# Optimization experiments

Hardware: AMD Instinct MI355X
Metric: run time of the kernel (lower is better)

Reference implementation:

```python
import jax, jax.numpy as jnp
import numpy as np
import math

B, T, C = 2, 2048, 1024
N_HEADS = 16  # config.head_size in the original (actually number of heads)
HEAD_DIM = C // N_HEADS


def setup_inputs() -> dict:
    key = jax.random.key(0)
    k1, k2, k3 = jax.random.split(key, 3)
    s = 1.0 / math.sqrt(C)
    return {
        "x": jax.random.normal(k1, (B, T, C), dtype=jnp.float32),
        "W_attn": jax.random.normal(k2, (C, 3 * C), dtype=jnp.float32) * s,
        "b_attn": jnp.zeros((3 * C,), dtype=jnp.float32),
        "W_proj": jax.random.normal(k3, (C, C), dtype=jnp.float32) * s,
        "b_proj": jnp.zeros((C,), dtype=jnp.float32),
    }


def reference(x, W_attn, b_attn, W_proj, b_proj):
    Bsz, Tlen, Cdim = x.shape
    qkv = x @ W_attn + b_attn                      # [B,T,3C]
    q, k, v = jnp.split(qkv, 3, axis=-1)
    # [B,T,C] -> [B,H,T,D]
    def to_heads(t):
        return t.reshape(Bsz, Tlen, N_HEADS, HEAD_DIM).transpose(0, 2, 1, 3)
    q, k, v = to_heads(q), to_heads(k), to_heads(v)
    # NOTE: original multiplies by sqrt(head_dim) (faithful to source, not 1/sqrt)
    scale = jnp.asarray(math.sqrt(HEAD_DIM), dtype=x.dtype)
    att = jnp.einsum("bhqd,bhkd->bhqk", q, k) * scale
    causal = jnp.tril(jnp.ones((Tlen, Tlen), dtype=bool))
    att = jnp.where(causal[None, None, :, :], att, jnp.asarray(-jnp.inf, x.dtype))
    att = jax.nn.softmax(att, axis=-1)
    # dropout layers are identity in eval mode
    y = jnp.einsum("bhqk,bhkd->bhqd", att, v)
    y = y.transpose(0, 2, 1, 3).reshape(Bsz, Tlen, Cdim)
    return y @ W_proj + b_proj
```

## Files before the change

### kernel.cpp

```cpp
#include <hip/hip_runtime.h>
#include <hip/hip_bf16.h>


#define B_  2
#define T_  2048
#define C_  1024
#define H_  16
#define D_  64
#define M_  (B_ * T_)
#define N3_ (3 * C_)

typedef __attribute__((ext_vector_type(8))) short s16x8;
typedef __attribute__((ext_vector_type(4))) short s16x4;
typedef __attribute__((ext_vector_type(4))) float f32x4;

typedef const __attribute__((address_space(1))) unsigned int gu32_t;
typedef __attribute__((address_space(3))) unsigned int lu32_t;

__device__ __forceinline__ void gload_lds16(const short* g, short* l) {
    __builtin_amdgcn_global_load_lds((gu32_t*)g, (lu32_t*)l, 16, 0, 0);
}

__device__ __forceinline__ float b2f(unsigned short u) {
    return __uint_as_float(((unsigned)u) << 16);
}
__device__ __forceinline__ unsigned short f2b(float f) {
    unsigned u = __float_as_uint(f);
    return (unsigned short)((u + 0x7FFFu + ((u >> 16) & 1u)) >> 16);
}
__device__ __forceinline__ float fexp2(float x) {
#if __has_builtin(__builtin_amdgcn_exp2f)
    return __builtin_amdgcn_exp2f(x);
#else
    return exp2f(x);
#endif
}

__global__ __launch_bounds__(256) void cvt_split(
    const float* __restrict__ in, short* __restrict__ oh, short* __restrict__ ol, int n)
{
    int i = (blockIdx.x * 256 + threadIdx.x) * 8;
    if (i >= n) return;
    float4 a = *(const float4*)&in[i];
    float4 b = *(const float4*)&in[i + 4];
    float v[8] = {a.x, a.y, a.z, a.w, b.x, b.y, b.z, b.w};
    s16x8 h, l;
    #pragma unroll
    for (int j = 0; j < 8; j++) {
        unsigned short hb = f2b(v[j]);
        h[j] = (short)hb;
        l[j] = (short)f2b(v[j] - b2f(hb));
    }
    *(s16x8*)&oh[i] = h;
    *(s16x8*)&ol[i] = l;
}

__global__ __launch_bounds__(256) void cvtT_split(
    const float* __restrict__ in, short* __restrict__ oh, short* __restrict__ ol,
    int R, int Cn)
{
    __shared__ short th[64][80];
    __shared__ short tl[64][80];
    const int tid = threadIdx.x;
    const int k0 = blockIdx.y * 64;
    const int n0 = blockIdx.x * 64;
    {
        int rl = tid >> 4, cl = (tid & 15) * 4;
        #pragma unroll
        for (int i = 0; i < 4; i++) {
            int kr = rl + i * 16;
            float4 v4 = *(const float4*)&in[(size_t)(k0 + kr) * Cn + n0 + cl];
            float v[4] = {v4.x, v4.y, v4.z, v4.w};
            #pragma unroll
            for (int j = 0; j < 4; j++) {
                unsigned short hb = f2b(v[j]);
                th[cl + j][kr] = (short)hb;
                tl[cl + j][kr] = (short)f2b(v[j] - b2f(hb));
            }
        }
    }
    __syncthreads();
    {
        int ro = tid >> 2, co = (tid & 3) * 16;
        *(s16x8*)&oh[(size_t)(n0 + ro) * R + k0 + co]     = *(s16x8*)&th[ro][co];
        *(s16x8*)&oh[(size_t)(n0 + ro) * R + k0 + co + 8] = *(s16x8*)&th[ro][co + 8];
        *(s16x8*)&ol[(size_t)(n0 + ro) * R + k0 + co]     = *(s16x8*)&tl[ro][co];
        *(s16x8*)&ol[(size_t)(n0 + ro) * R + k0 + co + 8] = *(s16x8*)&tl[ro][co + 8];
    }
}

__global__ __launch_bounds__(256) void cvtT_bf16(
    const float* __restrict__ in, short* __restrict__ out, int R, int Cn)
{
    __shared__ short t[64][80];
    const int tid = threadIdx.x;
    const int k0 = blockIdx.y * 64;
    const int n0 = blockIdx.x * 64;
    {
        int rl = tid >> 4, cl = (tid & 15) * 4;
        #pragma unroll
        for (int i = 0; i < 4; i++) {
            int kr = rl + i * 16;
            float4 v = *(const float4*)&in[(size_t)(k0 + kr) * Cn + n0 + cl];
            t[cl + 0][kr] = (short)f2b(v.x);
            t[cl + 1][kr] = (short)f2b(v.y);
            t[cl + 2][kr] = (short)f2b(v.z);
            t[cl + 3][kr] = (short)f2b(v.w);
        }
    }
    __syncthreads();
    {
        int ro = tid >> 2, co = (tid & 3) * 16;
        *(s16x8*)&out[(size_t)(n0 + ro) * R + k0 + co]     = *(s16x8*)&t[ro][co];
        *(s16x8*)&out[(size_t)(n0 + ro) * R + k0 + co + 8] = *(s16x8*)&t[ro][co + 8];
    }
}

__global__ __launch_bounds__(256) void qkv_qk(
    const short* __restrict__ Ah, const short* __restrict__ Al,
    const short* __restrict__ BTh, const short* __restrict__ BTl,
    const float* __restrict__ bias,
    short* __restrict__ Qh, short* __restrict__ Ql,
    short* __restrict__ Kh, short* __restrict__ Kl)
{
    __shared__ short Ash[128 * 32], Asl[128 * 32];
    __shared__ short Bsh[128 * 32], Bsl[128 * 32];

    const int tid  = threadIdx.x;
    const int wave = tid >> 6, lane = tid & 63;
    const int wm = wave >> 1, wn = wave & 1;
    const int lm = lane & 15, lq = lane >> 4;
    const int m0 = blockIdx.y * 128, n0 = blockIdx.x * 128;
    const int gr = (lane >> 2);
    const int gc = (lane & 3) * 8;

    f32x4 acc[4][4] = {};

    for (int k0 = 0; k0 < C_; k0 += 32) {
        __syncthreads();
        #pragma unroll
        for (int j = 0; j < 2; j++) {
            int s = wave * 2 + j;
            int row = s * 16 + gr;
            size_t ga = (size_t)(m0 + row) * C_ + k0 + gc;
            size_t gb = (size_t)(n0 + row) * C_ + k0 + gc;
            gload_lds16(&Ah[ga],  &Ash[s * 512]);
            gload_lds16(&Al[ga],  &Asl[s * 512]);
            gload_lds16(&BTh[gb], &Bsh[s * 512]);
            gload_lds16(&BTl[gb], &Bsl[s * 512]);
        }
        __syncthreads();

        s16x8 ah[4], al[4], bh[4], bl[4];
        #pragma unroll
        for (int mi = 0; mi < 4; mi++) {
            int r = wm * 64 + mi * 16 + lm;
            ah[mi] = *(const s16x8*)&Ash[r * 32 + lq * 8];
            al[mi] = *(const s16x8*)&Asl[r * 32 + lq * 8];
        }
        #pragma unroll
        for (int nj = 0; nj < 4; nj++) {
            int r = wn * 64 + nj * 16 + lm;
            bh[nj] = *(const s16x8*)&Bsh[r * 32 + lq * 8];
            bl[nj] = *(const s16x8*)&Bsl[r * 32 + lq * 8];
        }
        #pragma unroll
        for (int mi = 0; mi < 4; mi++)
            #pragma unroll
            for (int nj = 0; nj < 4; nj++) {
                acc[mi][nj] = __builtin_amdgcn_mfma_f32_16x16x32_bf16(
                    ah[mi], bh[nj], acc[mi][nj], 0, 0, 0);
                acc[mi][nj] = __builtin_amdgcn_mfma_f32_16x16x32_bf16(
                    ah[mi], bl[nj], acc[mi][nj], 0, 0, 0);
                acc[mi][nj] = __builtin_amdgcn_mfma_f32_16x16x32_bf16(
                    al[mi], bh[nj], acc[mi][nj], 0, 0, 0);
            }
    }

    #pragma unroll
    for (int nj = 0; nj < 4; nj++) {
        int n = n0 + wn * 64 + nj * 16 + lm;
        float bv = bias[n];
        int isK = n >> 10;
        int c = n & (C_ - 1);
        int h = c >> 6, d = c & (D_ - 1);
        short* dh = isK ? Kh : Qh;
        short* dl = isK ? Kl : Ql;
        float scale = isK ? 1.0f : 11.541560327111708f;
        #pragma unroll
        for (int mi = 0; mi < 4; mi++) {
            #pragma unroll
            for (int r = 0; r < 4; r++) {
                int m  = m0 + wm * 64 + mi * 16 + lq * 4 + r;
                int bb = m >> 11, t = m & (T_ - 1);
                float v = (acc[mi][nj][r] + bv) * scale;
                size_t idx = (((size_t)bb * H_ + h) * T_ + t) * D_ + d;
                unsigned short hb = f2b(v);
                dh[idx] = (short)hb;
                dl[idx] = (short)f2b(v - b2f(hb));
            }
        }
    }
}

__global__ __launch_bounds__(256) void qkv_v(
    const short* __restrict__ Ah, const short* __restrict__ BTh,
    const float* __restrict__ bias, short* __restrict__ VT)
{
    __shared__ short Ash[128 * 32];
    __shared__ short Bsh[128 * 32];

    const int tid  = threadIdx.x;
    const int wave = tid >> 6, lane = tid & 63;
    const int wm = wave >> 1, wn = wave & 1;
    const int lm = lane & 15, lq = lane >> 4;
    const int m0 = blockIdx.y * 128, n0 = blockIdx.x * 128;
    const int gr = (lane >> 2);
    const int gc = (lane & 3) * 8;

    f32x4 acc[4][4] = {};

    for (int k0 = 0; k0 < C_; k0 += 32) {
        __syncthreads();
        #pragma unroll
        for (int j = 0; j < 2; j++) {
            int s = wave * 2 + j;
            int row = s * 16 + gr;
            gload_lds16(&Ah[(size_t)(m0 + row) * C_ + k0 + gc],  &Ash[s * 512]);
            gload_lds16(&BTh[(size_t)(n0 + row) * C_ + k0 + gc], &Bsh[s * 512]);
        }
        __syncthreads();

        s16x8 af[4], bfr[4];
        #pragma unroll
        for (int mi = 0; mi < 4; mi++)
            af[mi] = *(const s16x8*)&Ash[(wm * 64 + mi * 16 + lm) * 32 + lq * 8];
        #pragma unroll
        for (int nj = 0; nj < 4; nj++)
            bfr[nj] = *(const s16x8*)&Bsh[(wn * 64 + nj * 16 + lm) * 32 + lq * 8];
        #pragma unroll
        for (int mi = 0; mi < 4; mi++)
            #pragma unroll
            for (int nj = 0; nj < 4; nj++)
                acc[mi][nj] = __builtin_amdgcn_mfma_f32_16x16x32_bf16(
                    af[mi], bfr[nj], acc[mi][nj], 0, 0, 0);
    }

    #pragma unroll
    for (int nj = 0; nj < 4; nj++) {
        int n = n0 + wn * 64 + nj * 16 + lm;
        float bv = bias[n];
        int h = n >> 6, d = n & (D_ - 1);
        #pragma unroll
        for (int mi = 0; mi < 4; mi++) {
            #pragma unroll
            for (int r = 0; r < 4; r++) {
                int m  = m0 + wm * 64 + mi * 16 + lq * 4 + r;
                int bb = m >> 11, t = m & (T_ - 1);
                VT[(((size_t)bb * H_ + h) * D_ + d) * T_ + t] =
                    (short)f2b(acc[mi][nj][r] + bv);
            }
        }
    }
}

__global__ __launch_bounds__(256) void proj_mfma(
    const short* __restrict__ A, const short* __restrict__ BT,
    const float* __restrict__ bias, float* __restrict__ out)
{
    __shared__ short Ash[128 * 32];
    __shared__ short Bsh[128 * 32];

    const int tid  = threadIdx.x;
    const int wave = tid >> 6, lane = tid & 63;
    const int wm = wave >> 1, wn = wave & 1;
    const int lm = lane & 15, lq = lane >> 4;
    const int m0 = blockIdx.y * 128, n0 = blockIdx.x * 128;
    const int gr = (lane >> 2);
    const int gc = (lane & 3) * 8;

    f32x4 acc[4][4] = {};

    for (int k0 = 0; k0 < C_; k0 += 32) {
        __syncthreads();
        #pragma unroll
        for (int j = 0; j < 2; j++) {
            int s = wave * 2 + j;
            int row = s * 16 + gr;
            gload_lds16(&A[(size_t)(m0 + row) * C_ + k0 + gc],  &Ash[s * 512]);
            gload_lds16(&BT[(size_t)(n0 + row) * C_ + k0 + gc], &Bsh[s * 512]);
        }
        __syncthreads();

        s16x8 af[4], bfr[4];
        #pragma unroll
        for (int mi = 0; mi < 4; mi++)
            af[mi] = *(const s16x8*)&Ash[(wm * 64 + mi * 16 + lm) * 32 + lq * 8];
        #pragma unroll
        for (int nj = 0; nj < 4; nj++)
            bfr[nj] = *(const s16x8*)&Bsh[(wn * 64 + nj * 16 + lm) * 32 + lq * 8];
        #pragma unroll
        for (int mi = 0; mi < 4; mi++)
            #pragma unroll
            for (int nj = 0; nj < 4; nj++)
                acc[mi][nj] = __builtin_amdgcn_mfma_f32_16x16x32_bf16(
                    af[mi], bfr[nj], acc[mi][nj], 0, 0, 0);
    }

    #pragma unroll
    for (int nj = 0; nj < 4; nj++) {
        int n = n0 + wn * 64 + nj * 16 + lm;
        float bv = bias[n];
        #pragma unroll
        for (int mi = 0; mi < 4; mi++) {
            #pragma unroll
            for (int r = 0; r < 4; r++) {
                int m = m0 + wm * 64 + mi * 16 + lq * 4 + r;
                out[(size_t)m * C_ + n] = acc[mi][nj][r] + bv;
            }
        }
    }
}

__global__ __launch_bounds__(256) void attn_mfma(
    const short* __restrict__ Qh, const short* __restrict__ Ql,
    const short* __restrict__ Kh, const short* __restrict__ Kl,
    const short* __restrict__ VT, short* __restrict__ Yb)
{
    __shared__ short Ksh[64][72], Ksl[64][72];
    __shared__ short Vt [64][72];
    __shared__ short Ps [4][16][72];

    const int tid  = threadIdx.x;
    const int wave = tid >> 6, lane = tid & 63;
    const int lm   = lane & 15, quad = lane >> 4;

    const int bid = blockIdx.x;
    const int xcd = bid & 7;
    const int r_  = bid >> 3;
    const int bhl = r_ & 3;
    const int u   = r_ >> 2;
    const int g_  = u >> 3, j_ = u & 7;
    const int qt  = (g_ == 0) ? j_ : (g_ == 1) ? 15 - j_
                  : (g_ == 2) ? 16 + j_ : 31 - j_;
    const int bh  = xcd * 4 + bhl;
    const int b   = bh >> 4, h = bh & (H_ - 1);
    const int q0  = qt * 64;
    const size_t base  = (size_t)bh * T_ * D_;
    const size_t vbase = (size_t)bh * D_ * T_;

    const int src = tid >> 3;
    const int sch = (tid & 7) * 8;

    #pragma unroll
    for (int i = 0; i < 2; i++) {
        int row = i * 32 + src;
        size_t gq = base + (size_t)(q0 + row) * D_ + sch;
        *(s16x8*)&Ksh[row][sch] = *(const s16x8*)&Qh[gq];
        *(s16x8*)&Ksl[row][sch] = *(const s16x8*)&Ql[gq];
    }
    __syncthreads();
    s16x8 bqh[2], bql[2];
    #pragma unroll
    for (int kc = 0; kc < 2; kc++) {
        bqh[kc] = *(const s16x8*)&Ksh[wave * 16 + lm][kc * 32 + quad * 8];
        bql[kc] = *(const s16x8*)&Ksl[wave * 16 + lm][kc * 32 + quad * 8];
    }

    s16x8 pkh[2], pkl[2], pvt[2];
    #pragma unroll
    for (int i = 0; i < 2; i++) {
        int row = i * 32 + src;
        size_t gk = base + (size_t)row * D_ + sch;
        pkh[i] = *(const s16x8*)&Kh[gk];
        pkl[i] = *(const s16x8*)&Kl[gk];
        pvt[i] = *(const s16x8*)&VT[vbase + (size_t)row * T_ + sch];
    }

    float mrow = -INFINITY, lrow = 0.f;
    f32x4 O[4] = {};

    for (int kt = 0; kt <= qt; kt++) {
        __syncthreads();
        #pragma unroll
        for (int i = 0; i < 2; i++) {
            int row = i * 32 + src;
            *(s16x8*)&Ksh[row][sch] = pkh[i];
            *(s16x8*)&Ksl[row][sch] = pkl[i];
            *(s16x8*)&Vt [row][sch] = pvt[i];
        }
        if (kt < qt) {
            #pragma unroll
            for (int i = 0; i < 2; i++) {
                int row = i * 32 + src;
                size_t gk = base + (size_t)((kt + 1) * 64 + row) * D_ + sch;
                pkh[i] = *(const s16x8*)&Kh[gk];
                pkl[i] = *(const s16x8*)&Kl[gk];
                pvt[i] = *(const s16x8*)&VT[vbase + (size_t)row * T_ + (kt + 1) * 64 + sch];
            }
        }
        __syncthreads();

        f32x4 S[4] = {};
        #pragma unroll
        for (int t = 0; t < 4; t++) {
            #pragma unroll
            for (int kc = 0; kc < 2; kc++) {
                s16x8 kh8 = *(const s16x8*)&Ksh[t * 16 + lm][kc * 32 + quad * 8];
                s16x8 kl8 = *(const s16x8*)&Ksl[t * 16 + lm][kc * 32 + quad * 8];
                S[t] = __builtin_amdgcn_mfma_f32_16x16x32_bf16(kh8, bqh[kc], S[t], 0, 0, 0);
                S[t] = __builtin_amdgcn_mfma_f32_16x16x32_bf16(kl8, bqh[kc], S[t], 0, 0, 0);
                S[t] = __builtin_amdgcn_mfma_f32_16x16x32_bf16(kh8, bql[kc], S[t], 0, 0, 0);
            }
        }

        const int qg = wave * 16 + lm;
        if (kt == qt) {
            #pragma unroll
            for (int t = 0; t < 4; t++)
                #pragma unroll
                for (int r = 0; r < 4; r++)
                    if ((t * 16 + quad * 4 + r) > qg) S[t][r] = -INFINITY;
        }

        float rm = -INFINITY;
        #pragma unroll
        for (int t = 0; t < 4; t++)
            #pragma unroll
            for (int r = 0; r < 4; r++) rm = fmaxf(rm, S[t][r]);
        rm = fmaxf(rm, __shfl_xor(rm, 16, 64));
        rm = fmaxf(rm, __shfl_xor(rm, 32, 64));
        float mnew  = fmaxf(mrow, rm);
        float alpha = fexp2(mrow - mnew);
        mrow = mnew;
        float rs = 0.f;
        #pragma unroll
        for (int t = 0; t < 4; t++)
            #pragma unroll
            for (int r = 0; r < 4; r++) {
                S[t][r] = fexp2(S[t][r] - mnew);
                rs += S[t][r];
            }
        rs += __shfl_xor(rs, 16, 64);
        rs += __shfl_xor(rs, 32, 64);
        lrow = lrow * alpha + rs;

        float al[4];
        #pragma unroll
        for (int r = 0; r < 4; r++) al[r] = __shfl(alpha, quad * 4 + r, 64);
        #pragma unroll
        for (int t = 0; t < 4; t++)
            #pragma unroll
            for (int r = 0; r < 4; r++) O[t][r] *= al[r];

        #pragma unroll
        for (int t = 0; t < 4; t++) {
            s16x4 p;
            #pragma unroll
            for (int r = 0; r < 4; r++)
                p[r] = (short)(__float_as_uint(S[t][r]) >> 16);
            *(s16x4*)&Ps[wave][lm][t * 16 + quad * 4] = p;
        }

        s16x8 ap[2];
        #pragma unroll
        for (int kc = 0; kc < 2; kc++)
            ap[kc] = *(const s16x8*)&Ps[wave][lm][kc * 32 + quad * 8];
        #pragma unroll
        for (int t = 0; t < 4; t++) {
            #pragma unroll
            for (int kc = 0; kc < 2; kc++) {
                s16x8 bv = *(const s16x8*)&Vt[t * 16 + lm][kc * 32 + quad * 8];
                O[t] = __builtin_amdgcn_mfma_f32_16x16x32_bf16(ap[kc], bv, O[t], 0, 0, 0);
            }
        }
    }

    float li[4];
    #pragma unroll
    for (int r = 0; r < 4; r++)
        li[r] = 1.0f / __shfl(lrow, quad * 4 + r, 64);
    #pragma unroll
    for (int t = 0; t < 4; t++)
        #pragma unroll
        for (int r = 0; r < 4; r++) {
            int q = q0 + wave * 16 + quad * 4 + r;
            int d = t * 16 + lm;
            Yb[((size_t)b * T_ + q) * C_ + h * D_ + d] =
                (short)f2b(O[t][r] * li[r]);
        }
}

extern "C" void kernel_launch(void* const* d_in, const int* in_sizes, int n_in,
                              void* d_out, int out_size, void* d_ws, size_t ws_size,
                              hipStream_t stream)
{
    const float* x      = (const float*)d_in[0];
    const float* W_attn = (const float*)d_in[1];
    const float* b_attn = (const float*)d_in[2];
    const float* W_proj = (const float*)d_in[3];
    const float* b_proj = (const float*)d_in[4];
    float* out = (float*)d_out;

    char* ws = (char*)d_ws;
    const size_t MB = 1024 * 1024;
    short* Qh   = (short*)(ws);
    short* Ql   = (short*)(ws +  8 * MB);
    short* Kh   = (short*)(ws + 16 * MB);
    short* Kl   = (short*)(ws + 24 * MB);
    short* xh   = (short*)(ws + 32 * MB);
    short* xl   = (short*)(ws + 40 * MB);
    short* WaTh = (short*)(ws + 48 * MB);
    short* WaTl = (short*)(ws + 54 * MB);
    short* WpT  = (short*)(ws + 60 * MB);
    short* VT   = (short*)(ws + 40 * MB);
    short* Yb   = (short*)(ws + 32 * MB);

    cvt_split <<<dim3(M_ * C_ / 2048), 256, 0, stream>>>(x, xh, xl, M_ * C_);
    cvtT_split<<<dim3(N3_ / 64, C_ / 64), 256, 0, stream>>>(W_attn, WaTh, WaTl, C_, N3_);
    cvtT_bf16 <<<dim3(C_ / 64, C_ / 64), 256, 0, stream>>>(W_proj, WpT, C_, C_);

    qkv_qk <<<dim3(16, 32), 256, 0, stream>>>(xh, xl, WaTh, WaTl, b_attn,
                                              Qh, Ql, Kh, Kl);
    qkv_v  <<<dim3(8, 32), 256, 0, stream>>>(xh, WaTh + (size_t)2048 * C_,
                                             b_attn + 2048, VT);
    attn_mfma<<<dim3(1024), 256, 0, stream>>>(Qh, Ql, Kh, Kl, VT, Yb);
    proj_mfma<<<dim3(8, 32), 256, 0, stream>>>(Yb, WpT, b_proj, out);
}
```

Baseline: 254.6 us.

## Split long causal attention tiles across two blocks and fuse prep kernels

Query tiles in the second half of the sequence now have their key range split between two blocks. Each block writes an unnormalised bf16 partial output plus its running max and sum, and a new merge kernel combines the two halves with log-sum-exp weights. This shortens the longest per-block work on the causal triangle and gives 1536 blocks instead of 1024, at the cost of an extra launch, partial-result traffic and bf16 rounding of the partials. Separately, the three input conversion and transpose kernels are merged into one launch that dispatches on block index, and the loop barrier is moved so the next-tile prefetch is issued after the LDS stores.

```diff
diff --git a/kernel.cpp b/kernel.cpp
--- a/kernel.cpp
+++ b/kernel.cpp
@@ -36,83 +36,85 @@
 #endif
 }
 
-__global__ __launch_bounds__(256) void cvt_split(
-    const float* __restrict__ in, short* __restrict__ oh, short* __restrict__ ol, int n)
-{
-    int i = (blockIdx.x * 256 + threadIdx.x) * 8;
-    if (i >= n) return;
-    float4 a = *(const float4*)&in[i];
-    float4 b = *(const float4*)&in[i + 4];
-    float v[8] = {a.x, a.y, a.z, a.w, b.x, b.y, b.z, b.w};
-    s16x8 h, l;
-    #pragma unroll
-    for (int j = 0; j < 8; j++) {
-        unsigned short hb = f2b(v[j]);
-        h[j] = (short)hb;
-        l[j] = (short)f2b(v[j] - b2f(hb));
-    }
-    *(s16x8*)&oh[i] = h;
-    *(s16x8*)&ol[i] = l;
-}
-
-__global__ __launch_bounds__(256) void cvtT_split(
-    const float* __restrict__ in, short* __restrict__ oh, short* __restrict__ ol,
-    int R, int Cn)
+__global__ __launch_bounds__(256) void prep(
+    const float* __restrict__ x,  short* __restrict__ xh, short* __restrict__ xl,
+    const float* __restrict__ Wa, short* __restrict__ WaTh, short* __restrict__ WaTl,
+    const float* __restrict__ Wp, short* __restrict__ WpT)
 {
     __shared__ short th[64][80];
     __shared__ short tl[64][80];
     const int tid = threadIdx.x;
-    const int k0 = blockIdx.y * 64;
-    const int n0 = blockIdx.x * 64;
+    const int bid = blockIdx.x;
+
+    if (bid < 2048) {
+        int i = (bid * 256 + tid) * 8;
+        float4 a = *(const float4*)&x[i];
+        float4 b = *(const float4*)&x[i + 4];
+        float v[8] = {a.x, a.y, a.z, a.w, b.x, b.y, b.z, b.w};
+        s16x8 h, l;
+        #pragma unroll
+        for (int j = 0; j < 8; j++) {
+            unsigned short hb = f2b(v[j]);
+            h[j] = (short)hb;
+            l[j] = (short)f2b(v[j] - b2f(hb));
+        }
+        *(s16x8*)&xh[i] = h;
+        *(s16x8*)&xl[i] = l;
+        return;
+    }
+
+    if (bid < 2816) {
+        int i2 = bid - 2048;
+        int bx = i2 % 48, by = i2 / 48;
+        int k0 = by * 64, n0 = bx * 64;
+        {
+            int rl = tid >> 4, cl = (tid & 15) * 4;
+            #pragma unroll
+            for (int i = 0; i < 4; i++) {
+                int kr = rl + i * 16;
+                float4 v4 = *(const float4*)&Wa[(size_t)(k0 + kr) * N3_ + n0 + cl];
+                float v[4] = {v4.x, v4.y, v4.z, v4.w};
+                #pragma unroll
+                for (int j = 0; j < 4; j++) {
+                    unsigned short hb = f2b(v[j]);
+                    th[cl + j][kr] = (short)hb;
+                    tl[cl + j][kr] = (short)f2b(v[j] - b2f(hb));
+                }
+            }
+        }
+        __syncthreads();
+        {
+            int ro = tid >> 2, co = (tid & 3) * 16;
+            *(s16x8*)&WaTh[(size_t)(n0 + ro) * C_ + k0 + co]     = *(s16x8*)&th[ro][co];
+            *(s16x8*)&WaTh[(size_t)(n0 + ro) * C_ + k0 + co + 8] = *(s16x8*)&th[ro][co + 8];
+            *(s16x8*)&WaTl[(size_t)(n0 + ro) * C_ + k0 + co]     = *(s16x8*)&tl[ro][co];
+            *(s16x8*)&WaTl[(size_t)(n0 + ro) * C_ + k0 + co + 8] = *(s16x8*)&tl[ro][co + 8];
+        }
+        return;
+    }
+
     {
-        int rl = tid >> 4, cl = (tid & 15) * 4;
-        #pragma unroll
-        for (int i = 0; i < 4; i++) {
-            int kr = rl + i * 16;
-            float4 v4 = *(const float4*)&in[(size_t)(k0 + kr) * Cn + n0 + cl];
-            float v[4] = {v4.x, v4.y, v4.z, v4.w};
-            #pragma unroll
-            for (int j = 0; j < 4; j++) {
-                unsigned short hb = f2b(v[j]);
-                th[cl + j][kr] = (short)hb;
-                tl[cl + j][kr] = (short)f2b(v[j] - b2f(hb));
-            }
-        }
-    }
-    __syncthreads();
-    {
-        int ro = tid >> 2, co = (tid & 3) * 16;
-        *(s16x8*)&oh[(size_t)(n0 + ro) * R + k0 + co]     = *(s16x8*)&th[ro][co];
-        *(s16x8*)&oh[(size_t)(n0 + ro) * R + k0 + co + 8] = *(s16x8*)&th[ro][co + 8];
-        *(s16x8*)&ol[(size_t)(n0 + ro) * R + k0 + co]     = *(s16x8*)&tl[ro][co];
-        *(s16x8*)&ol[(size_t)(n0 + ro) * R + k0 + co + 8] = *(s16x8*)&tl[ro][co + 8];
-    }
-}
-
-__global__ __launch_bounds__(256) void cvtT_bf16(
-    const float* __restrict__ in, short* __restrict__ out, int R, int Cn)
-{
-    __shared__ short t[64][80];
-    const int tid = threadIdx.x;
-    const int k0 = blockIdx.y * 64;
-    const int n0 = blockIdx.x * 64;
-    {
-        int rl = tid >> 4, cl = (tid & 15) * 4;
-        #pragma unroll
-        for (int i = 0; i < 4; i++) {
-            int kr = rl + i * 16;
-            float4 v = *(const float4*)&in[(size_t)(k0 + kr) * Cn + n0 + cl];
-            t[cl + 0][kr] = (short)f2b(v.x);
-            t[cl + 1][kr] = (short)f2b(v.y);
-            t[cl + 2][kr] = (short)f2b(v.z);
-            t[cl + 3][kr] = (short)f2b(v.w);
-        }
-    }
-    __syncthreads();
-    {
-        int ro = tid >> 2, co = (tid & 3) * 16;
-        *(s16x8*)&out[(size_t)(n0 + ro) * R + k0 + co]     = *(s16x8*)&t[ro][co];
-        *(s16x8*)&out[(size_t)(n0 + ro) * R + k0 + co + 8] = *(s16x8*)&t[ro][co + 8];
+        int i3 = bid - 2816;
+        int bx = i3 & 15, by = i3 >> 4;
+        int k0 = by * 64, n0 = bx * 64;
+        {
+            int rl = tid >> 4, cl = (tid & 15) * 4;
+            #pragma unroll
+            for (int i = 0; i < 4; i++) {
+                int kr = rl + i * 16;
+                float4 v = *(const float4*)&Wp[(size_t)(k0 + kr) * C_ + n0 + cl];
+                th[cl + 0][kr] = (short)f2b(v.x);
+                th[cl + 1][kr] = (short)f2b(v.y);
+                th[cl + 2][kr] = (short)f2b(v.z);
+                th[cl + 3][kr] = (short)f2b(v.w);
+            }
+        }
+        __syncthreads();
+        {
+            int ro = tid >> 2, co = (tid & 3) * 16;
+            *(s16x8*)&WpT[(size_t)(n0 + ro) * C_ + k0 + co]     = *(s16x8*)&th[ro][co];
+            *(s16x8*)&WpT[(size_t)(n0 + ro) * C_ + k0 + co + 8] = *(s16x8*)&th[ro][co + 8];
+        }
     }
 }
 
@@ -325,7 +327,8 @@
 __global__ __launch_bounds__(256) void attn_mfma(
     const short* __restrict__ Qh, const short* __restrict__ Ql,
     const short* __restrict__ Kh, const short* __restrict__ Kl,
-    const short* __restrict__ VT, short* __restrict__ Yb)
+    const short* __restrict__ VT, short* __restrict__ Yb,
+    short* __restrict__ Op, float2* __restrict__ ml)
 {
     __shared__ short Ksh[64][72], Ksl[64][72];
     __shared__ short Vt [64][72];
@@ -340,9 +343,16 @@
     const int r_  = bid >> 3;
     const int bhl = r_ & 3;
     const int u   = r_ >> 2;
-    const int g_  = u >> 3, j_ = u & 7;
-    const int qt  = (g_ == 0) ? j_ : (g_ == 1) ? 15 - j_
-                  : (g_ == 2) ? 16 + j_ : 31 - j_;
+    int qt, kt0, kt1, part;
+    if (u < 16) { qt = u; kt0 = 0; kt1 = qt; part = -1; }
+    else {
+        int idx = u - 16;
+        qt   = 16 + (idx >> 1);
+        part = idx & 1;
+        int halfk = (qt + 1) >> 1;
+        kt0 = part ? halfk : 0;
+        kt1 = part ? qt : halfk - 1;
+    }
     const int bh  = xcd * 4 + bhl;
     const int b   = bh >> 4, h = bh & (H_ - 1);
     const int q0  = qt * 64;
@@ -371,16 +381,16 @@
     #pragma unroll
     for (int i = 0; i < 2; i++) {
         int row = i * 32 + src;
-        size_t gk = base + (size_t)row * D_ + sch;
+        size_t gk = base + (size_t)(kt0 * 64 + row) * D_ + sch;
         pkh[i] = *(const s16x8*)&Kh[gk];
         pkl[i] = *(const s16x8*)&Kl[gk];
-        pvt[i] = *(const s16x8*)&VT[vbase + (size_t)row * T_ + sch];
+        pvt[i] = *(const s16x8*)&VT[vbase + (size_t)row * T_ + kt0 * 64 + sch];
     }
 
     float mrow = -INFINITY, lrow = 0.f;
     f32x4 O[4] = {};
 
-    for (int kt = 0; kt <= qt; kt++) {
+    for (int kt = kt0; kt <= kt1; kt++) {
         __syncthreads();
         #pragma unroll
         for (int i = 0; i < 2; i++) {
@@ -389,7 +399,8 @@
             *(s16x8*)&Ksl[row][sch] = pkl[i];
             *(s16x8*)&Vt [row][sch] = pvt[i];
         }
-        if (kt < qt) {
+        __syncthreads();
+        if (kt < kt1) {
             #pragma unroll
             for (int i = 0; i < 2; i++) {
                 int row = i * 32 + src;
@@ -399,7 +410,6 @@
                 pvt[i] = *(const s16x8*)&VT[vbase + (size_t)row * T_ + (kt + 1) * 64 + sch];
             }
         }
-        __syncthreads();
 
         f32x4 S[4] = {};
         #pragma unroll
@@ -476,19 +486,66 @@
         }
     }
 
-    float li[4];
-    #pragma unroll
-    for (int r = 0; r < 4; r++)
-        li[r] = 1.0f / __shfl(lrow, quad * 4 + r, 64);
-    #pragma unroll
-    for (int t = 0; t < 4; t++)
-        #pragma unroll
-        for (int r = 0; r < 4; r++) {
-            int q = q0 + wave * 16 + quad * 4 + r;
-            int d = t * 16 + lm;
-            Yb[((size_t)b * T_ + q) * C_ + h * D_ + d] =
-                (short)f2b(O[t][r] * li[r]);
-        }
+    if (part < 0) {
+        float li[4];
+        #pragma unroll
+        for (int r = 0; r < 4; r++)
+            li[r] = 1.0f / __shfl(lrow, quad * 4 + r, 64);
+        #pragma unroll
+        for (int t = 0; t < 4; t++)
+            #pragma unroll
+            for (int r = 0; r < 4; r++) {
+                int q = q0 + wave * 16 + quad * 4 + r;
+                int d = t * 16 + lm;
+                Yb[((size_t)b * T_ + q) * C_ + h * D_ + d] =
+                    (short)f2b(O[t][r] * li[r]);
+            }
+    } else {
+        size_t obase = ((size_t)part * 32 + bh) * 1024 * 64;
+        #pragma unroll
+        for (int t = 0; t < 4; t++)
+            #pragma unroll
+            for (int r = 0; r < 4; r++) {
+                int ql = (q0 - 1024) + wave * 16 + quad * 4 + r;
+                int d  = t * 16 + lm;
+                Op[obase + (size_t)ql * 64 + d] = (short)f2b(O[t][r]);
+            }
+        if (quad == 0) {
+            int ql = (q0 - 1024) + wave * 16 + lm;
+            ml[((size_t)part * 32 + bh) * 1024 + ql] = make_float2(mrow, lrow);
+        }
+    }
+}
+
+__global__ __launch_bounds__(256) void attn_merge(
+    const short* __restrict__ Op, const float2* __restrict__ ml,
+    short* __restrict__ Yb)
+{
+    int eid = blockIdx.x * 256 + threadIdx.x;
+    int dc  = eid & 7;
+    int ql  = (eid >> 3) & 1023;
+    int bh  = eid >> 13;
+    int b   = bh >> 4, h = bh & (H_ - 1);
+
+    float2 m0l = ml[(size_t)bh * 1024 + ql];
+    float2 m1l = ml[(size_t)(32 + bh) * 1024 + ql];
+    float mm = fmaxf(m0l.x, m1l.x);
+    float a0 = fexp2(m0l.x - mm);
+    float a1 = fexp2(m1l.x - mm);
+    float inv = 1.0f / (m0l.y * a0 + m1l.y * a1);
+    a0 *= inv; a1 *= inv;
+
+    size_t ob = ((size_t)bh * 1024 + ql) * 64 + dc * 8;
+    s16x8 o0 = *(const s16x8*)&Op[ob];
+    s16x8 o1 = *(const s16x8*)&Op[(size_t)32 * 1024 * 64 + ob];
+    s16x8 y;
+    #pragma unroll
+    for (int j = 0; j < 8; j++)
+        y[j] = (short)f2b(b2f((unsigned short)o0[j]) * a0 +
+                          b2f((unsigned short)o1[j]) * a1);
+
+    int q = 1024 + ql;
+    *(s16x8*)&Yb[((size_t)b * T_ + q) * C_ + h * D_ + dc * 8] = y;
 }
 
 extern "C" void kernel_launch(void* const* d_in, const int* in_sizes, int n_in,
@@ -504,26 +561,27 @@
 
     char* ws = (char*)d_ws;
     const size_t MB = 1024 * 1024;
-    short* Qh   = (short*)(ws);
-    short* Ql   = (short*)(ws +  8 * MB);
-    short* Kh   = (short*)(ws + 16 * MB);
-    short* Kl   = (short*)(ws + 24 * MB);
-    short* xh   = (short*)(ws + 32 * MB);
-    short* xl   = (short*)(ws + 40 * MB);
-    short* WaTh = (short*)(ws + 48 * MB);
-    short* WaTl = (short*)(ws + 54 * MB);
-    short* WpT  = (short*)(ws + 60 * MB);
-    short* VT   = (short*)(ws + 40 * MB);
-    short* Yb   = (short*)(ws + 32 * MB);
-
-    cvt_split <<<dim3(M_ * C_ / 2048), 256, 0, stream>>>(x, xh, xl, M_ * C_);
-    cvtT_split<<<dim3(N3_ / 64, C_ / 64), 256, 0, stream>>>(W_attn, WaTh, WaTl, C_, N3_);
-    cvtT_bf16 <<<dim3(C_ / 64, C_ / 64), 256, 0, stream>>>(W_proj, WpT, C_, C_);
-
-    qkv_qk <<<dim3(16, 32), 256, 0, stream>>>(xh, xl, WaTh, WaTl, b_attn,
-                                              Qh, Ql, Kh, Kl);
-    qkv_v  <<<dim3(8, 32), 256, 0, stream>>>(xh, WaTh + (size_t)2048 * C_,
-                                             b_attn + 2048, VT);
-    attn_mfma<<<dim3(1024), 256, 0, stream>>>(Qh, Ql, Kh, Kl, VT, Yb);
-    proj_mfma<<<dim3(8, 32), 256, 0, stream>>>(Yb, WpT, b_proj, out);
-}
+    short*  Qh   = (short*)(ws);
+    short*  Ql   = (short*)(ws +  8 * MB);
+    short*  Kh   = (short*)(ws + 16 * MB);
+    short*  Kl   = (short*)(ws + 24 * MB);
+    short*  xh   = (short*)(ws + 32 * MB);
+    short*  xl   = (short*)(ws + 40 * MB);
+    short*  WaTh = (short*)(ws + 48 * MB);
+    short*  WaTl = (short*)(ws + 54 * MB);
+    short*  WpT  = (short*)(ws + 60 * MB);
+    short*  VT   = (short*)(ws + 40 * MB);
+    short*  Yb   = (short*)(ws + 32 * MB);
+    short*  Op   = (short*)(ws + 48 * MB);
+    float2* ml   = (float2*)(ws + 56 * MB);
+
+    prep  <<<dim3(3072), 256, 0, stream>>>(x, xh, xl, W_attn, WaTh, WaTl,
+                                           W_proj, WpT);
+    qkv_qk<<<dim3(16, 32), 256, 0, stream>>>(xh, xl, WaTh, WaTl, b_attn,
+                                             Qh, Ql, Kh, Kl);
+    qkv_v <<<dim3(8, 32), 256, 0, stream>>>(xh, WaTh + (size_t)2048 * C_,
+                                            b_attn + 2048, VT);
+    attn_mfma <<<dim3(1536), 256, 0, stream>>>(Qh, Ql, Kh, Kl, VT, Yb, Op, ml);
+    attn_merge<<<dim3(1024), 256, 0, stream>>>(Op, ml, Yb);
+    proj_mfma <<<dim3(8, 32), 256, 0, stream>>>(Yb, WpT, b_proj, out);
+}
```

After: 264.9 us. 4.1% more time.
